# Kernel tuning notes

Hardware: AMD Instinct MI355X
Metric: run time of the kernel (lower is better)

Reference implementation:

```python
import jax, jax.numpy as jnp
import numpy as np

L = 768
Z_DIM = 128
C = 32
EPS = 1e-5


def _layer_norm(x, w, b):
    mu = jnp.mean(x, axis=-1, keepdims=True)
    var = jnp.mean(jnp.square(x - mu), axis=-1, keepdims=True)
    return (x - mu) * jax.lax.rsqrt(var + EPS) * w + b


def setup_inputs() -> dict:
    key = jax.random.key(0)
    ks = jax.random.split(key, 12)
    s_z = 1.0 / np.sqrt(Z_DIM)
    s_c = 1.0 / np.sqrt(C)
    return {
        "z": jax.random.normal(ks[0], (L, L, Z_DIM), dtype=jnp.float32),
        "norm_w": jnp.ones((Z_DIM,), jnp.float32),
        "norm_b": jnp.zeros((Z_DIM,), jnp.float32),
        "onorm_w": jnp.ones((C,), jnp.float32),
        "onorm_b": jnp.zeros((C,), jnp.float32),
        "a_w": jax.random.normal(ks[1], (C, Z_DIM), jnp.float32) * s_z,
        "a_b": jnp.zeros((C,), jnp.float32),
        "ag_w": jax.random.normal(ks[2], (C, Z_DIM), jnp.float32) * s_z,
        "ag_b": jnp.zeros((C,), jnp.float32),
        "g_w": jax.random.normal(ks[3], (Z_DIM, Z_DIM), jnp.float32) * s_z,
        "g_b": jnp.zeros((Z_DIM,), jnp.float32),
        "o_w": jax.random.normal(ks[4], (Z_DIM, C), jnp.float32) * s_c,
        "o_b": jnp.zeros((Z_DIM,), jnp.float32),
    }


def reference(z, norm_w, norm_b, onorm_w, onorm_b, a_w, a_b, ag_w, ag_b, g_w, g_b, o_w, o_b):
    zn = _layer_norm(z, norm_w, norm_b)                       # [L,L,Z]
    a = (zn @ a_w.T + a_b) * jax.nn.sigmoid(zn @ ag_w.T + ag_b)  # [L,L,C]
    # source computes b with the same (a) projections -> b == a
    o = jnp.einsum('ilc,jlc->ijc', a, a)                      # [L,L,C]
    o = _layer_norm(o, onorm_w, onorm_b)
    o = o @ o_w.T + o_b                                        # [L,L,Z]
    o = o * jax.nn.sigmoid(zn @ g_w.T + g_b)
    return o
```

## Files before the change

### kernel.cpp

```cpp
#include <hip/hip_runtime.h>
#include <math.h>


#define LDIM 768
#define LL   (768 * 768)
#define ZD   128
#define CD   32

typedef __bf16 bf16x8 __attribute__((ext_vector_type(8)));
typedef float  f32x4  __attribute__((ext_vector_type(4)));

__device__ __forceinline__ ushort f2bf(float f) {
    __bf16 h = (__bf16)f;
    return __builtin_bit_cast(ushort, h);
}
__device__ __forceinline__ float bf2f(ushort u) {
    return __builtin_bit_cast(float, ((unsigned)u) << 16);
}
__device__ __forceinline__ float sigm(float x) {
    return __builtin_amdgcn_rcpf(1.0f + __expf(-x));
}

__global__ __launch_bounds__(256) void k0_wfrag(
    const float* __restrict__ aw, const float* __restrict__ agw,
    const float* __restrict__ gw, const float* __restrict__ ow,
    ushort* __restrict__ wfrag, ushort* __restrict__ ofrag)
{
    const int idx = blockIdx.x * 256 + threadIdx.x;
    if (idx >= 3584) return;
    union { ushort us[8]; uint4 q; } pk;
    if (idx < 3072) {
        const int f = idx, n4 = f >> 6, lane = f & 63;
        const int n = n4 >> 2, kk = n4 & 3;
        const int fr = lane & 15, hi = lane >> 4;
        const int ch = n * 16 + fr;
        const int k0 = kk * 32 + hi * 8;
        const float* src = (ch < 32) ? (aw + ch * ZD)
                         : (ch < 64) ? (agw + (ch - 32) * ZD)
                                     : (gw + (ch - 64) * ZD);
        #pragma unroll
        for (int j = 0; j < 8; ++j) pk.us[j] = f2bf(src[k0 + j]);
        *(uint4*)&wfrag[(size_t)f * 8] = pk.q;
    } else {
        const int e = idx - 3072;
        const int n = e >> 6, lane = e & 63;
        const int fr = lane & 15, hi = lane >> 4;
        const float* src = ow + (n * 16 + fr) * CD + hi * 8;
        #pragma unroll
        for (int j = 0; j < 8; ++j) pk.us[j] = f2bf(src[j]);
        *(uint4*)&ofrag[(size_t)e * 8] = pk.q;
    }
}

__global__ __launch_bounds__(256) void k1_ln_proj(
    const float* __restrict__ z, const float* __restrict__ nw, const float* __restrict__ nb,
    const ushort* __restrict__ wfrag,
    const float* __restrict__ ab, const float* __restrict__ agb, const float* __restrict__ gb,
    ushort* __restrict__ a_t, ushort* __restrict__ gate)
{
    __shared__ ushort zn[64][136];
    __shared__ ushort gl[64][136];

    const int tid = threadIdx.x;
    const int lane = tid & 63, wave = tid >> 6;
    const int fr = lane & 15, hi = lane >> 4;

    const int t0 = (wave < 2) ? wave     : 6 + (wave - 2) * 3;
    const int t1 = (wave < 2) ? wave + 2 : t0 + 1;
    const int t2 = (wave < 2) ? wave + 4 : t0 + 2;

    bf16x8 bv0[4], bv1[4], bv2[4];
    {
        const ushort* wl = wfrag + (size_t)lane * 8;
        #pragma unroll
        for (int kk = 0; kk < 4; ++kk) {
            bv0[kk] = *(const bf16x8*)(wl + (size_t)(t0 * 4 + kk) * 512);
            bv1[kk] = *(const bf16x8*)(wl + (size_t)(t1 * 4 + kk) * 512);
            bv2[kk] = *(const bf16x8*)(wl + (size_t)(t2 * 4 + kk) * 512);
        }
    }

    float abv = 0.f, agbv = 0.f, gbv0 = 0.f, gbv1 = 0.f, gbv2;
    if (wave < 2) {
        abv  = ab[wave * 16 + fr];
        agbv = agb[wave * 16 + fr];
        gbv2 = gb[t2 * 16 - 64 + fr];
    } else {
        gbv0 = gb[t0 * 16 - 64 + fr];
        gbv1 = gb[t1 * 16 - 64 + fr];
        gbv2 = gb[t2 * 16 - 64 + fr];
    }

    const size_t blockrow = (size_t)blockIdx.x * 256;
    const int lr = tid >> 2, seg = tid & 3;

    float4 zreg[8];
    {
        const float4* zp = (const float4*)(z + (blockrow + lr) * ZD + seg * 32);
        #pragma unroll
        for (int q = 0; q < 8; ++q) zreg[q] = zp[q];
    }

    auto copy_out = [&](int cc) {
        const size_t rbp = blockrow + (size_t)cc * 64;
        #pragma unroll
        for (int it = 0; it < 4; ++it) {
            const int idx = it * 256 + tid;
            const int r = idx >> 4, cq = idx & 15;
            *(uint4*)&gate[(rbp + r) * ZD + cq * 8] = *(const uint4*)&gl[r][cq * 8];
        }
    };

    for (int c = 0; c < 4; ++c) {
        __syncthreads();

        {
            float v[32];
            #pragma unroll
            for (int q = 0; q < 8; ++q) {
                v[q * 4 + 0] = zreg[q].x; v[q * 4 + 1] = zreg[q].y;
                v[q * 4 + 2] = zreg[q].z; v[q * 4 + 3] = zreg[q].w;
            }
            float s = 0.f, ss = 0.f;
            #pragma unroll
            for (int e = 0; e < 32; ++e) { s += v[e]; ss += v[e] * v[e]; }
            s += __shfl_xor(s, 1); ss += __shfl_xor(ss, 1);
            s += __shfl_xor(s, 2); ss += __shfl_xor(ss, 2);
            const float mu  = s * (1.f / 128.f);
            const float var = ss * (1.f / 128.f) - mu * mu;
            const float rs  = rsqrtf(var + 1e-5f);
            union { ushort u[32]; uint4 q4[4]; } pk;
            #pragma unroll
            for (int e = 0; e < 32; ++e) {
                const int k = seg * 32 + e;
                pk.u[e] = f2bf((v[e] - mu) * rs * nw[k] + nb[k]);
            }
            #pragma unroll
            for (int q = 0; q < 4; ++q)
                *(uint4*)&zn[lr][seg * 32 + q * 8] = pk.q4[q];
        }

        if (c > 0) copy_out(c - 1);

        if (c < 3) {
            const float4* zp = (const float4*)(z + (blockrow + (c + 1) * 64 + lr) * ZD + seg * 32);
            #pragma unroll
            for (int q = 0; q < 8; ++q) zreg[q] = zp[q];
        }
        __syncthreads();

        f32x4 acc0[4], acc1[4], acc2[4];
        #pragma unroll
        for (int m = 0; m < 4; ++m) {
            acc0[m] = (f32x4){0.f, 0.f, 0.f, 0.f};
            acc1[m] = (f32x4){0.f, 0.f, 0.f, 0.f};
            acc2[m] = (f32x4){0.f, 0.f, 0.f, 0.f};
        }
        #pragma unroll
        for (int m = 0; m < 4; ++m) {
            bf16x8 afm[4];
            #pragma unroll
            for (int kk = 0; kk < 4; ++kk)
                afm[kk] = *(const bf16x8*)&zn[m * 16 + fr][kk * 32 + hi * 8];
            #pragma unroll
            for (int kk = 0; kk < 4; ++kk) {
                acc0[m] = __builtin_amdgcn_mfma_f32_16x16x32_bf16(afm[kk], bv0[kk], acc0[m], 0, 0, 0);
                acc1[m] = __builtin_amdgcn_mfma_f32_16x16x32_bf16(afm[kk], bv1[kk], acc1[m], 0, 0, 0);
                acc2[m] = __builtin_amdgcn_mfma_f32_16x16x32_bf16(afm[kk], bv2[kk], acc2[m], 0, 0, 0);
            }
        }

        const size_t rb = blockrow + (size_t)c * 64;
        if (wave < 2) {
            const int ch = wave * 16 + fr;
            #pragma unroll
            for (int m = 0; m < 4; ++m) {
                union { ushort u[4]; uint2 d; } pk;
                #pragma unroll
                for (int q = 0; q < 4; ++q)
                    pk.u[q] = f2bf((acc0[m][q] + abv) * sigm(acc1[m][q] + agbv));
                *(uint2*)&a_t[(size_t)ch * LL + rb + m * 16 + hi * 4] = pk.d;
            }
            const int gch = t2 * 16 - 64 + fr;
            #pragma unroll
            for (int m = 0; m < 4; ++m)
                #pragma unroll
                for (int q = 0; q < 4; ++q)
                    gl[m * 16 + hi * 4 + q][gch] = f2bf(sigm(acc2[m][q] + gbv2));
        } else {
            const int g0 = t0 * 16 - 64 + fr;
            const int g1 = t1 * 16 - 64 + fr;
            const int g2 = t2 * 16 - 64 + fr;
            #pragma unroll
            for (int m = 0; m < 4; ++m)
                #pragma unroll
                for (int q = 0; q < 4; ++q) {
                    const int row = m * 16 + hi * 4 + q;
                    gl[row][g0] = f2bf(sigm(acc0[m][q] + gbv0));
                    gl[row][g1] = f2bf(sigm(acc1[m][q] + gbv1));
                    gl[row][g2] = f2bf(sigm(acc2[m][q] + gbv2));
                }
        }
    }
    __syncthreads();
    copy_out(3);
}

__global__ __launch_bounds__(256) void k2_einsum(
    const ushort* __restrict__ a_t, ushort* __restrict__ obuf16)
{
    __shared__ ushort As[2][128][32];
    __shared__ ushort Bs[2][128][32];

    const int tid = threadIdx.x;
    const int c = blockIdx.y;
    int p = blockIdx.x, bi = 0;
    while (p >= 6 - bi) { p -= 6 - bi; ++bi; }
    const int bj = bi + p;
    const int i0 = bi * 128, j0 = bj * 128;
    const ushort* base = a_t + (size_t)c * LL;

    const int wave = tid >> 6, lane = tid & 63;
    const int wr = (wave >> 1) * 64, wc = (wave & 1) * 64;
    const int fr = lane & 15, hi = lane >> 4, k8 = hi * 8;

    f32x4 acc[4][4];
    #pragma unroll
    for (int m = 0; m < 4; ++m)
        #pragma unroll
        for (int n = 0; n < 4; ++n)
            acc[m][n] = (f32x4){0.f, 0.f, 0.f, 0.f};

    auto stage = [&](int b, int kc) {
        #pragma unroll
        for (int i = 0; i < 2; ++i) {
            const int idx = i * 256 + tid;
            const int row = idx >> 2, sc = (idx & 3) * 8;
            __builtin_amdgcn_global_load_lds(
                (const uint*)(base + (size_t)(i0 + row) * LDIM + kc * 32 + sc),
                (uint*)&As[b][row][sc], 16, 0, 0);
            __builtin_amdgcn_global_load_lds(
                (const uint*)(base + (size_t)(j0 + row) * LDIM + kc * 32 + sc),
                (uint*)&Bs[b][row][sc], 16, 0, 0);
        }
    };

    stage(0, 0);
    __syncthreads();
    for (int kc = 0; kc < 24; ++kc) {
        const int cur = kc & 1;
        if (kc + 1 < 24) stage(cur ^ 1, kc + 1);

        bf16x8 av[4], bv[4];
        #pragma unroll
        for (int m = 0; m < 4; ++m)
            av[m] = *(const bf16x8*)&As[cur][wr + m * 16 + fr][k8];
        #pragma unroll
        for (int n = 0; n < 4; ++n)
            bv[n] = *(const bf16x8*)&Bs[cur][wc + n * 16 + fr][k8];

        #pragma unroll
        for (int m = 0; m < 4; ++m)
            #pragma unroll
            for (int n = 0; n < 4; ++n)
                acc[m][n] = __builtin_amdgcn_mfma_f32_16x16x32_bf16(
                    av[m], bv[n], acc[m][n], 0, 0, 0);
        __syncthreads();
    }

    ushort* ob = obuf16 + (size_t)c * LL;
    #pragma unroll
    for (int m = 0; m < 4; ++m)
        #pragma unroll
        for (int n = 0; n < 4; ++n) {
            #pragma unroll
            for (int q = 0; q < 4; ++q) {
                const int row = i0 + wr + m * 16 + hi * 4 + q;
                const int col = j0 + wc + n * 16 + fr;
                ob[(size_t)row * LDIM + col] = f2bf(acc[m][n][q]);
            }
            if (bi != bj) {
                const int mrow = j0 + wc + n * 16 + fr;
                const int mcol = i0 + wr + m * 16 + hi * 4;
                union { ushort u[4]; uint2 d; } pk;
                #pragma unroll
                for (int q = 0; q < 4; ++q) pk.u[q] = f2bf(acc[m][n][q]);
                *(uint2*)&ob[(size_t)mrow * LDIM + mcol] = pk.d;
            }
        }
}

__global__ __launch_bounds__(256) void k3_out(
    const ushort* __restrict__ obuf16,
    const float* __restrict__ onw, const float* __restrict__ onb,
    const ushort* __restrict__ ofrag, const float* __restrict__ obias,
    const ushort* __restrict__ gate, float* __restrict__ out)
{
    __shared__ union { float Ol[64][40]; float Res[64][132]; } u;
    __shared__ ushort An[64][36];

    const int tid = threadIdx.x;
    const int lane = tid & 63, wave = tid >> 6;
    const size_t rowbase = (size_t)blockIdx.x * 64;

    bf16x8 ofr[8];
    #pragma unroll
    for (int n = 0; n < 8; ++n)
        ofr[n] = *(const bf16x8*)&ofrag[(size_t)n * 512 + lane * 8];

    #pragma unroll
    for (int cc = 0; cc < 4; ++cc) {
        const int ch = wave * 8 + cc * 2 + (lane >> 5);
        const int r2 = (lane & 31) * 2;
        const uint uu = *(const uint*)&obuf16[(size_t)ch * LL + rowbase + r2];
        u.Ol[r2][ch]     = bf2f((ushort)(uu & 0xffff));
        u.Ol[r2 + 1][ch] = bf2f((ushort)(uu >> 16));
    }
    __syncthreads();

    {
        const int r = tid >> 2, seg = tid & 3;
        float v[8];
        #pragma unroll
        for (int e = 0; e < 8; ++e) v[e] = u.Ol[r][seg * 8 + e];
        float s = 0.f, ss = 0.f;
        #pragma unroll
        for (int e = 0; e < 8; ++e) { s += v[e]; ss += v[e] * v[e]; }
        s += __shfl_xor(s, 1); ss += __shfl_xor(ss, 1);
        s += __shfl_xor(s, 2); ss += __shfl_xor(ss, 2);
        const float mu  = s * (1.f / 32.f);
        const float var = ss * (1.f / 32.f) - mu * mu;
        const float rs  = rsqrtf(var + 1e-5f);
        union { ushort us[8]; uint4 q; } pk;
        #pragma unroll
        for (int e = 0; e < 8; ++e) {
            const int c = seg * 8 + e;
            pk.us[e] = f2bf((v[e] - mu) * rs * onw[c] + onb[c]);
        }
        *(uint4*)&An[r][seg * 8] = pk.q;
    }
    __syncthreads();

    const int fr = lane & 15, hi = lane >> 4;
    const int wrow = wave * 16;

    const bf16x8 af = *(const bf16x8*)&An[wrow + fr][hi * 8];
    f32x4 acc[8];
    #pragma unroll
    for (int n = 0; n < 8; ++n)
        acc[n] = __builtin_amdgcn_mfma_f32_16x16x32_bf16(
            af, ofr[n], (f32x4){0.f, 0.f, 0.f, 0.f}, 0, 0, 0);

    #pragma unroll
    for (int n = 0; n < 8; ++n) {
        const int ch = n * 16 + fr;
        const float obv = obias[ch];
        #pragma unroll
        for (int q = 0; q < 4; ++q)
            u.Res[wrow + hi * 4 + q][ch] = acc[n][q] + obv;
    }
    __syncthreads();

    #pragma unroll
    for (int it = 0; it < 8; ++it) {
        const int idx = it * 256 + tid;
        const int r = idx >> 5, cq = (idx & 31) * 4;
        float4 v4 = *(const float4*)&u.Res[r][cq];
        union { uint2 d; ushort us[4]; } g;
        g.d = *(const uint2*)&gate[(rowbase + r) * ZD + cq];
        v4.x *= bf2f(g.us[0]); v4.y *= bf2f(g.us[1]);
        v4.z *= bf2f(g.us[2]); v4.w *= bf2f(g.us[3]);
        *(float4*)&out[(rowbase + r) * ZD + cq] = v4;
    }
}

extern "C" void kernel_launch(void* const* d_in, const int* in_sizes, int n_in,
                              void* d_out, int out_size, void* d_ws, size_t ws_size,
                              hipStream_t stream) {
    (void)in_sizes; (void)n_in; (void)out_size; (void)ws_size;
    const float* z   = (const float*)d_in[0];
    const float* nw  = (const float*)d_in[1];
    const float* nb  = (const float*)d_in[2];
    const float* onw = (const float*)d_in[3];
    const float* onb = (const float*)d_in[4];
    const float* aw  = (const float*)d_in[5];
    const float* ab  = (const float*)d_in[6];
    const float* agw = (const float*)d_in[7];
    const float* agb = (const float*)d_in[8];
    const float* gw  = (const float*)d_in[9];
    const float* gb  = (const float*)d_in[10];
    const float* ow  = (const float*)d_in[11];
    const float* ob  = (const float*)d_in[12];

    char* ws = (char*)d_ws;
    ushort* a_t    = (ushort*)ws;
    ushort* gate   = (ushort*)(ws + 37748736);
    ushort* obuf16 = (ushort*)(ws + 188743680);
    ushort* wfrag  = (ushort*)(ws + 226492416);
    ushort* ofrag  = (ushort*)(ws + 226541568);

    k0_wfrag<<<14, 256, 0, stream>>>(aw, agw, gw, ow, wfrag, ofrag);
    k1_ln_proj<<<LL / 256, 256, 0, stream>>>(z, nw, nb, wfrag, ab, agb, gb,
                                             a_t, gate);
    k2_einsum<<<dim3(21, 32), 256, 0, stream>>>(a_t, obuf16);
    k3_out<<<LL / 64, 256, 0, stream>>>(obuf16, onw, onb, ofrag, ob, gate,
                                        (float*)d_out);
}
```

Before: 262.2 us.

## Swizzle einsum block order and make output kernel wave-local with bf16 LDS

The einsum kernel now remaps linear block IDs so that consecutive blocks spread across channels, which is meant to improve L2/cache locality or balance. The output kernel stores intermediates in bf16 in shared memory and restructures the layernorm and epilogue so each wave handles only its own 16 rows. This replaces two block-wide barriers with lgkmcnt waits and shrinks shared memory. In exchange, the result is rounded to bf16 before gating, which costs accuracy.

```diff
diff --git a/kernel.cpp b/kernel.cpp
--- a/kernel.cpp
+++ b/kernel.cpp
@@ -213,8 +213,10 @@
     __shared__ ushort Bs[2][128][32];
 
     const int tid = threadIdx.x;
-    const int c = blockIdx.y;
-    int p = blockIdx.x, bi = 0;
+    const int lid = blockIdx.y * 21 + blockIdx.x;
+    const int swz = (lid & 7) * 84 + (lid >> 3);
+    const int c = swz / 21;
+    int p = swz % 21, bi = 0;
     while (p >= 6 - bi) { p -= 6 - bi; ++bi; }
     const int bj = bi + p;
     const int i0 = bi * 128, j0 = bj * 128;
@@ -296,12 +298,15 @@
     const ushort* __restrict__ ofrag, const float* __restrict__ obias,
     const ushort* __restrict__ gate, float* __restrict__ out)
 {
-    __shared__ union { float Ol[64][40]; float Res[64][132]; } u;
-    __shared__ ushort An[64][36];
+    __shared__ ushort Ol[64][40];
+    __shared__ ushort An[64][40];
+    __shared__ ushort Res[64][136];
 
     const int tid = threadIdx.x;
     const int lane = tid & 63, wave = tid >> 6;
+    const int fr = lane & 15, hi = lane >> 4;
     const size_t rowbase = (size_t)blockIdx.x * 64;
+    const int wrow = wave * 16;
 
     bf16x8 ofr[8];
     #pragma unroll
@@ -313,16 +318,18 @@
         const int ch = wave * 8 + cc * 2 + (lane >> 5);
         const int r2 = (lane & 31) * 2;
         const uint uu = *(const uint*)&obuf16[(size_t)ch * LL + rowbase + r2];
-        u.Ol[r2][ch]     = bf2f((ushort)(uu & 0xffff));
-        u.Ol[r2 + 1][ch] = bf2f((ushort)(uu >> 16));
+        Ol[r2][ch]     = (ushort)(uu & 0xffff);
+        Ol[r2 + 1][ch] = (ushort)(uu >> 16);
     }
     __syncthreads();
 
     {
-        const int r = tid >> 2, seg = tid & 3;
+        const int r = wrow + (lane >> 2), seg = lane & 3;
+        union { uint4 q; ushort us[8]; } raw;
+        raw.q = *(const uint4*)&Ol[r][seg * 8];
         float v[8];
         #pragma unroll
-        for (int e = 0; e < 8; ++e) v[e] = u.Ol[r][seg * 8 + e];
+        for (int e = 0; e < 8; ++e) v[e] = bf2f(raw.us[e]);
         float s = 0.f, ss = 0.f;
         #pragma unroll
         for (int e = 0; e < 8; ++e) { s += v[e]; ss += v[e] * v[e]; }
@@ -339,10 +346,7 @@
         }
         *(uint4*)&An[r][seg * 8] = pk.q;
     }
-    __syncthreads();
-
-    const int fr = lane & 15, hi = lane >> 4;
-    const int wrow = wave * 16;
+    asm volatile("s_waitcnt lgkmcnt(0)" ::: "memory");
 
     const bf16x8 af = *(const bf16x8*)&An[wrow + fr][hi * 8];
     f32x4 acc[8];
@@ -357,20 +361,23 @@
         const float obv = obias[ch];
         #pragma unroll
         for (int q = 0; q < 4; ++q)
-            u.Res[wrow + hi * 4 + q][ch] = acc[n][q] + obv;
-    }
-    __syncthreads();
+            Res[wrow + hi * 4 + q][ch] = f2bf(acc[n][q] + obv);
+    }
+    asm volatile("s_waitcnt lgkmcnt(0)" ::: "memory");
 
     #pragma unroll
     for (int it = 0; it < 8; ++it) {
-        const int idx = it * 256 + tid;
-        const int r = idx >> 5, cq = (idx & 31) * 4;
-        float4 v4 = *(const float4*)&u.Res[r][cq];
-        union { uint2 d; ushort us[4]; } g;
-        g.d = *(const uint2*)&gate[(rowbase + r) * ZD + cq];
-        v4.x *= bf2f(g.us[0]); v4.y *= bf2f(g.us[1]);
-        v4.z *= bf2f(g.us[2]); v4.w *= bf2f(g.us[3]);
-        *(float4*)&out[(rowbase + r) * ZD + cq] = v4;
+        const int r = wrow + it * 2 + (lane >> 5);
+        const int ch = (lane & 31) * 4;
+        union { uint2 d; ushort us[4]; } rv, g;
+        rv.d = *(const uint2*)&Res[r][ch];
+        g.d  = *(const uint2*)&gate[(rowbase + r) * ZD + ch];
+        float4 w;
+        w.x = bf2f(rv.us[0]) * bf2f(g.us[0]);
+        w.y = bf2f(rv.us[1]) * bf2f(g.us[1]);
+        w.z = bf2f(rv.us[2]) * bf2f(g.us[2]);
+        w.w = bf2f(rv.us[3]) * bf2f(g.us[3]);
+        *(float4*)&out[(rowbase + r) * ZD + ch] = w;
     }
 }
 
```

Result: faster. 255.6 us (median of 3 runs) (-2.5%).
